# Performance work log

Hardware: AMD Instinct MI355X
Metric: run time of the kernel (lower is better)

## Reference

```python
import jax, jax.numpy as jnp
import numpy as np

B, N1, N2 = 4, 2048, 8192
F_IN, F_OUT = 256, 256
K = 3          # PyG knn_interpolate default
BN_EPS = 1e-5


def linear_bn(x, W, b, gamma, beta):
    # Linear + BatchNorm1d (training mode: batch stats over B*N per feature)
    h = jnp.einsum('bni,io->bno', x, W) + b
    mean = h.mean(axis=(0, 1))
    var = h.var(axis=(0, 1))
    xhat = (h - mean) * jax.lax.rsqrt(var + BN_EPS)
    return gamma * xhat + beta


def knn_interpolate(f1, p1, p2):
    # f1: [N1,F], p1: [N1,3], p2: [N2,3] -> [N2,F]
    d2 = jnp.sum((p2[:, None, :] - p1[None, :, :]) ** 2, axis=-1)  # [N2,N1]
    neg_d2, idx = jax.lax.top_k(-d2, K)                            # k smallest
    w = 1.0 / jnp.maximum(-neg_d2, 1e-16)                          # [N2,K]
    fk = f1[idx]                                                   # [N2,K,F]
    return jnp.sum(w[..., None] * fk, axis=1) / jnp.sum(w, axis=1, keepdims=True)


def setup_inputs() -> dict:
    key = jax.random.key(0)
    ks = jax.random.split(key, 10)
    return {
        'features_1': jax.random.normal(ks[0], (B, N1, F_IN), jnp.float32),
        'positions_1': jax.random.uniform(ks[1], (B, N1, 3), jnp.float32),
        'batch_1': jnp.repeat(jnp.arange(B, dtype=jnp.int64), N1),
        'features_2': jax.random.normal(ks[2], (B, N2, F_IN), jnp.float32),
        'positions_2': jax.random.uniform(ks[3], (B, N2, 3), jnp.float32),
        'batch_2': jnp.repeat(jnp.arange(B, dtype=jnp.int64), N2),
        'W1': jax.random.normal(ks[4], (F_IN, F_OUT), jnp.float32) * (1.0 / np.sqrt(F_IN)),
        'b1': jax.random.normal(ks[5], (F_OUT,), jnp.float32) * 0.02,
        'gamma1': jnp.ones((F_OUT,), jnp.float32),
        'beta1': jnp.zeros((F_OUT,), jnp.float32),
        'W2': jax.random.normal(ks[6], (F_IN, F_OUT), jnp.float32) * (1.0 / np.sqrt(F_IN)),
        'b2': jax.random.normal(ks[7], (F_OUT,), jnp.float32) * 0.02,
        'gamma2': jnp.ones((F_OUT,), jnp.float32),
        'beta2': jnp.zeros((F_OUT,), jnp.float32),
    }


def reference(features_1, positions_1, batch_1, features_2, positions_2, batch_2,
              W1, b1, gamma1, beta1, W2, b2, gamma2, beta2):
    f1 = linear_bn(features_1, W1, b1, gamma1, beta1)          # [B,N1,F_OUT]
    f2 = linear_bn(features_2, W2, b2, gamma2, beta2)          # [B,N2,F_OUT]
    # batch structure is regular [B,N]: knn restricted within batch == vmap over B
    interp = jax.vmap(knn_interpolate)(f1, positions_1, positions_2)  # [B,N2,F_OUT]
    return (interp + f2, positions_2, batch_2)
```

## Files before the change

### kernel.cpp

```cpp
#include <hip/hip_runtime.h>
#include <math.h>

#define BATCH   4
#define N1      2048
#define N2      8192
#define F       256
#define NTOT1   (BATCH * N1)
#define NTOT2   (BATCH * N2)
#define BN_EPS  1e-5f

#define GR      6
#define NC      216
#define NCP     (NC + 1)
#define GH      (1.0f / 6.0f)

typedef __attribute__((ext_vector_type(8))) short bf16x8;
typedef __attribute__((ext_vector_type(8))) unsigned short u16x8;
typedef __attribute__((ext_vector_type(4))) float f32x4;

__device__ __forceinline__ unsigned short f2bf(float f) {
    unsigned u = __float_as_uint(f);
    unsigned r = (u + 0x7fffu + ((u >> 16) & 1u)) >> 16;
    return (unsigned short)r;
}
__device__ __forceinline__ float bflo(unsigned u) {
    return __uint_as_float(u << 16);
}
__device__ __forceinline__ float bfhi(unsigned u) {
    return __uint_as_float(u & 0xffff0000u);
}
__device__ __forceinline__ void async16(const void* g, void* l) {
    __builtin_amdgcn_global_load_lds(
        (const __attribute__((address_space(1))) unsigned int*)g,
        (__attribute__((address_space(3))) unsigned int*)l, 16, 0, 0);
}

__device__ __forceinline__ void ins3m(float d, int j,
                                      float& d0, float& d1, float& d2,
                                      int& j0, int& j1, int& j2) {
    const bool c0 = d < d0;
    const bool c1 = d < d1;
    const bool c2 = d < d2;
    const float nd1 = __builtin_amdgcn_fmed3f(d, d0, d1);
    const float nd2 = __builtin_amdgcn_fmed3f(d, d1, d2);
    d0 = fminf(d, d0);
    d1 = nd1;
    d2 = nd2;
    j2 = c1 ? j1 : (c2 ? j : j2);
    j1 = c0 ? j0 : (c1 ? j : j1);
    j0 = c0 ? j  : j0;
}

__device__ __forceinline__ int clamp6(int c) { return c < 0 ? 0 : (c > 5 ? 5 : c); }
__device__ __forceinline__ int cell_of(float x, float y, float z) {
    const int cx = clamp6((int)(x * 6.0f));
    const int cy = clamp6((int)(y * 6.0f));
    const int cz = clamp6((int)(z * 6.0f));
    return (cz * 6 + cy) * 6 + cx;
}

__global__ __launch_bounds__(256) void prep_kernel(const float* __restrict__ W1,
                                                   const float* __restrict__ W2,
                                                   unsigned short* __restrict__ Wt1,
                                                   unsigned short* __restrict__ Wt2,
                                                   float* __restrict__ sums) {
    const int bx = blockIdx.x;
    const int t  = threadIdx.x;

    if (bx < 32) {
        __shared__ float tile[64][65];
        const bool second = bx >= 16;
        const int bl = second ? bx - 16 : bx;
        const float* W = second ? W2 : W1;
        unsigned short* Wt = second ? Wt2 : Wt1;
        const int gx0 = (bl & 3) * 64;
        const int gy0 = (bl >> 2) * 64;
        const int tx = t & 63;
        const int ty = t >> 6;
        #pragma unroll
        for (int j = 0; j < 16; ++j) {
            const int row = ty * 16 + j;
            tile[row][tx] = W[(size_t)(gy0 + row) * 256 + gx0 + tx];
        }
        __syncthreads();
        #pragma unroll
        for (int j = 0; j < 16; ++j) {
            const int row = ty * 16 + j;
            Wt[(size_t)(gx0 + row) * 256 + gy0 + tx] = f2bf(tile[tx][row]);
        }
    } else {
        #pragma unroll
        for (int i = 0; i < 4; ++i) sums[t + 256 * i] = 0.0f;
    }
}

__global__ __launch_bounds__(256) void gemm_mfma_kernel(const float* __restrict__ f1,
                                                        const float* __restrict__ f2,
                                                        const unsigned short* __restrict__ Wt1,
                                                        const unsigned short* __restrict__ Wt2,
                                                        const float* __restrict__ b1,
                                                        const float* __restrict__ b2,
                                                        const float* __restrict__ p1,
                                                        const float* __restrict__ p2,
                                                        unsigned short* __restrict__ h1b,
                                                        unsigned short* __restrict__ h2b,
                                                        float* __restrict__ sums,
                                                        float4* __restrict__ gridPts,
                                                        int* __restrict__ cellStart,
                                                        int* __restrict__ qSorted,
                                                        int* __restrict__ qCellStart) {
    __shared__ unsigned short As[128 * 32];
    __shared__ unsigned short Bs[128 * 32];

    const int bx = blockIdx.x;
    const int t  = threadIdx.x;

    if (bx >= 640) {
        __shared__ int cnt[NC];
        __shared__ int ofs[NCP];
        __shared__ unsigned char cellb[N2];
        const int bb = bx - 640;
        if (bb < 4) {
            const int b = bb;
            if (t < NC) cnt[t] = 0;
            __syncthreads();
            int   myc[8];
            float mx[8], my[8], mz[8];
            #pragma unroll
            for (int r = 0; r < 8; ++r) {
                const int i = r * 256 + t;
                const size_t base = (size_t)(b * N1 + i) * 3;
                mx[r] = p1[base]; my[r] = p1[base + 1]; mz[r] = p1[base + 2];
                myc[r] = cell_of(mx[r], my[r], mz[r]);
                atomicAdd(&cnt[myc[r]], 1);
            }
            __syncthreads();
            if (t <= NC) ofs[t] = (t == 0) ? 0 : cnt[t - 1];
            __syncthreads();
            for (int dd = 1; dd < NCP; dd <<= 1) {
                int v = 0;
                if (t <= NC && t >= dd) v = ofs[t - dd];
                __syncthreads();
                if (t <= NC && t >= dd) ofs[t] += v;
                __syncthreads();
            }
            if (t < NC) cnt[t] = ofs[t];
            __syncthreads();
            #pragma unroll
            for (int r = 0; r < 8; ++r) {
                const int i = r * 256 + t;
                const int pos = atomicAdd(&cnt[myc[r]], 1);
                float4 rec;
                rec.x = mx[r]; rec.y = my[r]; rec.z = mz[r];
                rec.w = __int_as_float(i);
                gridPts[(size_t)b * N1 + pos] = rec;
            }
            if (t <= NC) cellStart[b * NCP + t] = ofs[t];
        } else {
            const int b = bb - 4;
            if (t < NC) cnt[t] = 0;
            __syncthreads();
            for (int r = 0; r < 32; ++r) {
                const int i = r * 256 + t;
                const size_t base = (size_t)(b * N2 + i) * 3;
                const int c = cell_of(p2[base], p2[base + 1], p2[base + 2]);
                cellb[i] = (unsigned char)c;
                atomicAdd(&cnt[c], 1);
            }
            __syncthreads();
            if (t <= NC) ofs[t] = (t == 0) ? 0 : cnt[t - 1];
            __syncthreads();
            for (int dd = 1; dd < NCP; dd <<= 1) {
                int v = 0;
                if (t <= NC && t >= dd) v = ofs[t - dd];
                __syncthreads();
                if (t <= NC && t >= dd) ofs[t] += v;
                __syncthreads();
            }
            if (t < NC) cnt[t] = ofs[t];
            __syncthreads();
            for (int r = 0; r < 32; ++r) {
                const int i = r * 256 + t;
                const int c = cellb[i];
                const int pos = atomicAdd(&cnt[c], 1);
                qSorted[(size_t)b * N2 + pos] = b * N2 + i;
            }
            if (t <= NC) qCellStart[b * NCP + t] = ofs[t];
        }
        return;
    }

    const int L  = (bx & 7) * 80 + (bx >> 3);
    const bool g2 = L >= 128;
    const int ll  = g2 ? L - 128 : L;
    const int mb  = ll >> 1;
    const int nbi = ll & 1;

    const float* Fsrc        = g2 ? f2 : f1;
    const unsigned short* Wt = g2 ? Wt2 : Wt1;
    const float* bias        = g2 ? b2 : b1;
    unsigned short* Hb       = g2 ? h2b : h1b;
    float* sum               = sums + (g2 ? 512 : 0);
    float* sumsq             = sum + 256;
    const int row0 = mb * 128;
    const int n0   = nbi * 128;

    const int wave = t >> 6;
    const int lane = t & 63;
    const int wm   = (wave & 1) * 64;
    const int wn   = (wave >> 1) * 64;
    const int ml   = lane & 15;
    const int q    = lane >> 4;

    float4 arA[2], arB[2];
    auto loadA = [&](int kt) {
        #pragma unroll
        for (int i = 0; i < 2; ++i) {
            const int pi  = i * 256 + t;
            const int row = pi >> 2;
            const int q2  = pi & 3;
            const float4* src = (const float4*)Fsrc
                              + (size_t)(row0 + row) * 64 + kt * 8 + q2 * 2;
            arA[i] = src[0];
            arB[i] = src[1];
        }
    };
    auto writeA = [&]() {
        #pragma unroll
        for (int i = 0; i < 2; ++i) {
            const int pi  = i * 256 + t;
            const int row = pi >> 2;
            const int q2  = pi & 3;
            u16x8 v;
            v[0] = f2bf(arA[i].x); v[1] = f2bf(arA[i].y);
            v[2] = f2bf(arA[i].z); v[3] = f2bf(arA[i].w);
            v[4] = f2bf(arB[i].x); v[5] = f2bf(arB[i].y);
            v[6] = f2bf(arB[i].z); v[7] = f2bf(arB[i].w);
            *(u16x8*)&As[row * 32 + q2 * 8] = v;
        }
    };
    auto stageB = [&](int kt) {
        #pragma unroll
        for (int r = 0; r < 2; ++r) {
            const int e   = r * 2048 + t * 8;
            const int row = e >> 5;
            const int kk  = e & 31;
            async16(Wt + (size_t)(n0 + row) * 256 + kt * 32 + kk,
                    (unsigned short*)Bs + e);
        }
    };

    f32x4 acc[4][4] = {};

    loadA(0);
    stageB(0);
    writeA();
    loadA(1);
    __syncthreads();

    for (int kt = 0; kt < 8; ++kt) {
        bf16x8 af[4], bfr[4];
        #pragma unroll
        for (int mt = 0; mt < 4; ++mt)
            af[mt] = *(const bf16x8*)&As[(wm + mt * 16 + ml) * 32 + q * 8];
        #pragma unroll
        for (int nt = 0; nt < 4; ++nt)
            bfr[nt] = *(const bf16x8*)&Bs[(wn + nt * 16 + ml) * 32 + q * 8];
        #pragma unroll
        for (int mt = 0; mt < 4; ++mt)
            #pragma unroll
            for (int nt = 0; nt < 4; ++nt)
                acc[mt][nt] = __builtin_amdgcn_mfma_f32_16x16x32_bf16(af[mt], bfr[nt],
                                                                      acc[mt][nt], 0, 0, 0);
        if (kt < 7) {
            __syncthreads();
            stageB(kt + 1);
            writeA();
            if (kt < 6) loadA(kt + 2);
            __syncthreads();
        }
    }

    float bv[4], psum[4], psq[4];
    #pragma unroll
    for (int nt = 0; nt < 4; ++nt) {
        bv[nt] = bias[n0 + wn + nt * 16 + ml];
        psum[nt] = 0.0f; psq[nt] = 0.0f;
    }
    #pragma unroll
    for (int mt = 0; mt < 4; ++mt)
        #pragma unroll
        for (int nt = 0; nt < 4; ++nt)
            #pragma unroll
            for (int r = 0; r < 4; ++r) {
                const float v = acc[mt][nt][r] + bv[nt];
                const int grow = row0 + wm + mt * 16 + q * 4 + r;
                Hb[(size_t)grow * 256 + n0 + wn + nt * 16 + ml] = f2bf(v);
                psum[nt] += v;
                psq[nt]  = fmaf(v, v, psq[nt]);
            }
    #pragma unroll
    for (int nt = 0; nt < 4; ++nt) {
        psum[nt] += __shfl_xor(psum[nt], 16, 64);
        psum[nt] += __shfl_xor(psum[nt], 32, 64);
        psq[nt]  += __shfl_xor(psq[nt], 16, 64);
        psq[nt]  += __shfl_xor(psq[nt], 32, 64);
    }
    if (q == 0) {
        #pragma unroll
        for (int nt = 0; nt < 4; ++nt) {
            const int col = n0 + wn + nt * 16 + ml;
            atomicAdd(&sum[col],   psum[nt]);
            atomicAdd(&sumsq[col], psq[nt]);
        }
    }
}

__global__ __launch_bounds__(512) void fused_kernel(const float* __restrict__ p2,
                                                    const unsigned short* __restrict__ h1b,
                                                    const unsigned short* __restrict__ h2b,
                                                    const float* __restrict__ sums,
                                                    const float* __restrict__ g1,
                                                    const float* __restrict__ be1,
                                                    const float* __restrict__ g2,
                                                    const float* __restrict__ be2,
                                                    const float4* __restrict__ gridPts,
                                                    const int* __restrict__ cellStart,
                                                    const int* __restrict__ qSorted,
                                                    const int* __restrict__ qCellStart,
                                                    float* __restrict__ out) {
    __shared__ float ssl[4][256];
    __shared__ int   cst[NCP];
    __shared__ float pdl[8][64][3];
    __shared__ int   pil[8][64][3];
    __shared__ float qdl[64][3];
    __shared__ int   qjl[64][3];
    __shared__ float wql[64][3];
    __shared__ int   jql[64][3];
    __shared__ int   qidl[64];
    __shared__ float qpx[64], qpy[64], qpz[64];

    const int t    = threadIdx.x;
    const int bx   = blockIdx.x;
    const int b    = bx / NC;
    const int cid  = bx - b * NC;
    const int ccx  = cid % 6;
    const int ccy  = (cid / 6) % 6;
    const int ccz  = cid / 36;
    const int wave = t >> 6;
    const int lane = t & 63;

    if (t < 256) {
        const float m1 = sums[t] * (1.0f / (float)NTOT1);
        const float v1 = sums[256 + t] * (1.0f / (float)NTOT1) - m1 * m1;
        const float s1 = g1[t] * rsqrtf(v1 + BN_EPS);
        ssl[0][t] = s1;
        ssl[1][t] = be1[t] - m1 * s1;
        const float m2 = sums[512 + t] * (1.0f / (float)NTOT2);
        const float v2 = sums[768 + t] * (1.0f / (float)NTOT2) - m2 * m2;
        const float s2 = g2[t] * rsqrtf(v2 + BN_EPS);
        ssl[2][t] = s2;
        ssl[3][t] = be2[t] - m2 * s2;
    }
    if (t < NCP) cst[t] = cellStart[b * NCP + t];

    const int qs = qCellStart[b * NCP + cid];
    const int qe = qCellStart[b * NCP + cid + 1];
    const float4* __restrict__ gp = gridPts + (size_t)b * N1;

    for (int q0 = qs; q0 < qe; q0 += 64) {
        const int nqc = min(64, qe - q0);
        __syncthreads();
        if (t < 64) {
            int qid = 0;
            float x = 1e30f, y = 1e30f, z = 1e30f;
            if (t < nqc) {
                qid = qSorted[(size_t)b * N2 + q0 + t];
                const size_t pb = (size_t)qid * 3;
                x = p2[pb]; y = p2[pb + 1]; z = p2[pb + 2];
            }
            qidl[t] = qid;
            qpx[t] = x; qpy[t] = y; qpz[t] = z;
        }
        __syncthreads();

        const float qx = qpx[lane], qy = qpy[lane], qz = qpz[lane];

        auto scan_box = [&](int R, float& d0, float& d1, float& d2,
                            int& i0, int& i1, int& i2) {
            const int dim  = 2 * R + 1;
            const int dim2 = dim * dim;
            const int nsl  = dim2 * dim;
            for (int sl = wave; sl < nsl; sl += 8) {
                int lz = sl / dim2;
                const int rem = sl - lz * dim2;
                int ly = rem / dim;
                int lx = rem - ly * dim;
                lx -= R; ly -= R; lz -= R;
                if (R > 1) {
                    const int ax = lx < 0 ? -lx : lx;
                    const int ay = ly < 0 ? -ly : ly;
                    const int az = lz < 0 ? -lz : lz;
                    int ch = ax > ay ? ax : ay;
                    ch = ch > az ? ch : az;
                    if (ch < R) continue;
                }
                const int gx = ccx + lx;
                const int gy = ccy + ly;
                const int gz = ccz + lz;
                if ((unsigned)gx >= 6u || (unsigned)gy >= 6u || (unsigned)gz >= 6u)
                    continue;
                const int cc = (gz * 6 + gy) * 6 + gx;
                const int s = __builtin_amdgcn_readfirstlane(cst[cc]);
                const int e = __builtin_amdgcn_readfirstlane(cst[cc + 1]);
                for (int j = s; j < e; ++j) {
                    const float4 p = gp[j];
                    const float dx = p.x - qx;
                    const float dy = p.y - qy;
                    const float dz = p.z - qz;
                    float d = dx * dx;
                    d = fmaf(dy, dy, d);
                    d = fmaf(dz, dz, d);
                    ins3m(d, __float_as_int(p.w), d0, d1, d2, i0, i1, i2);
                }
            }
        };

        auto merge_check = [&](int R) -> int {
            int notdone = 0;
            if (t < 64) {
                float m0, m1, m2;
                int a0, a1, a2;
                if (R == 1) { m0 = m1 = m2 = 1e30f; a0 = a1 = a2 = 0; }
                else {
                    m0 = qdl[t][0]; m1 = qdl[t][1]; m2 = qdl[t][2];
                    a0 = qjl[t][0]; a1 = qjl[t][1]; a2 = qjl[t][2];
                }
                #pragma unroll
                for (int s = 0; s < 8; ++s)
                    #pragma unroll
                    for (int k = 0; k < 3; ++k)
                        ins3m(pdl[s][t][k], pil[s][t][k], m0, m1, m2, a0, a1, a2);
                qdl[t][0] = m0; qdl[t][1] = m1; qdl[t][2] = m2;
                qjl[t][0] = a0; qjl[t][1] = a1; qjl[t][2] = a2;
                if (t < nqc) {
                    float dmin = 1e30f;
                    {
                        const int lo = ccx - R, hi = ccx + R;
                        if (lo > 0) dmin = fminf(dmin, qpx[t] - (float)lo * GH);
                        if (hi < 5) dmin = fminf(dmin, (float)(hi + 1) * GH - qpx[t]);
                    }
                    {
                        const int lo = ccy - R, hi = ccy + R;
                        if (lo > 0) dmin = fminf(dmin, qpy[t] - (float)lo * GH);
                        if (hi < 5) dmin = fminf(dmin, (float)(hi + 1) * GH - qpy[t]);
                    }
                    {
                        const int lo = ccz - R, hi = ccz + R;
                        if (lo > 0) dmin = fminf(dmin, qpz[t] - (float)lo * GH);
                        if (hi < 5) dmin = fminf(dmin, (float)(hi + 1) * GH - qpz[t]);
                    }
                    if (m2 > dmin * dmin * 0.9999f) notdone = 1;
                }
            }
            return __syncthreads_count(notdone);
        };

        {
            float d0 = 1e30f, d1 = 1e30f, d2 = 1e30f;
            int i0 = 0, i1 = 0, i2 = 0;
            scan_box(1, d0, d1, d2, i0, i1, i2);
            pdl[wave][lane][0] = d0; pdl[wave][lane][1] = d1; pdl[wave][lane][2] = d2;
            pil[wave][lane][0] = i0; pil[wave][lane][1] = i1; pil[wave][lane][2] = i2;
        }
        __syncthreads();
        int need = merge_check(1);
        for (int R = 2; need != 0 && R <= 6; ++R) {
            float d0 = 1e30f, d1 = 1e30f, d2 = 1e30f;
            int i0 = 0, i1 = 0, i2 = 0;
            scan_box(R, d0, d1, d2, i0, i1, i2);
            pdl[wave][lane][0] = d0; pdl[wave][lane][1] = d1; pdl[wave][lane][2] = d2;
            pil[wave][lane][0] = i0; pil[wave][lane][1] = i1; pil[wave][lane][2] = i2;
            __syncthreads();
            need = merge_check(R);
        }

        if (t < nqc) {
            const float w0 = 1.0f / fmaxf(qdl[t][0], 1e-16f);
            const float w1 = 1.0f / fmaxf(qdl[t][1], 1e-16f);
            const float w2 = 1.0f / fmaxf(qdl[t][2], 1e-16f);
            const float inv = 1.0f / (w0 + w1 + w2);
            wql[t][0] = w0 * inv; wql[t][1] = w1 * inv; wql[t][2] = w2 * inv;
            jql[t][0] = b * N1 + qjl[t][0];
            jql[t][1] = b * N1 + qjl[t][1];
            jql[t][2] = b * N1 + qjl[t][2];
        }
        __syncthreads();

        {
            const int fp = t & 127;
            const int f0 = fp * 2;
            const float s1a = ssl[0][f0],     t1a = ssl[1][f0];
            const float s2a = ssl[2][f0],     t2a = ssl[3][f0];
            const float s1b = ssl[0][f0 + 1], t1b = ssl[1][f0 + 1];
            const float s2b = ssl[2][f0 + 1], t2b = ssl[3][f0 + 1];
            for (int v = t >> 7; v < nqc; v += 4) {
                const int qid = qidl[v];
                const int   j0 = jql[v][0], j1 = jql[v][1], j2 = jql[v][2];
                const float w0 = wql[v][0], w1 = wql[v][1], w2 = wql[v][2];

                const unsigned u0 = *(const unsigned*)(h1b + (size_t)j0 * F + f0);
                const unsigned u1 = *(const unsigned*)(h1b + (size_t)j1 * F + f0);
                const unsigned u2 = *(const unsigned*)(h1b + (size_t)j2 * F + f0);
                const unsigned uh = *(const unsigned*)(h2b + (size_t)qid * F + f0);

                float alo = w0 * bflo(u0);
                alo = fmaf(w1, bflo(u1), alo);
                alo = fmaf(w2, bflo(u2), alo);
                float ahi = w0 * bfhi(u0);
                ahi = fmaf(w1, bfhi(u1), ahi);
                ahi = fmaf(w2, bfhi(u2), ahi);

                float2 o;
                o.x = fmaf(alo, s1a, t1a) + fmaf(bflo(uh), s2a, t2a);
                o.y = fmaf(ahi, s1b, t1b) + fmaf(bfhi(uh), s2b, t2b);
                *(float2*)(out + (size_t)qid * F + f0) = o;
            }
        }
    }

    if (t < 152) {
        const int tid = bx * 152 + t;
        if (tid < NTOT2 * 3) {
            out[(size_t)NTOT2 * F + tid] = p2[tid];
        } else if (tid < NTOT2 * 3 + NTOT2) {
            const int e = tid - NTOT2 * 3;
            out[(size_t)NTOT2 * F + NTOT2 * 3 + e] = (float)(e >> 13);
        }
    }
}

extern "C" void kernel_launch(void* const* d_in, const int* in_sizes, int n_in,
                              void* d_out, int out_size, void* d_ws, size_t ws_size,
                              hipStream_t stream) {
    const float* f1  = (const float*)d_in[0];
    const float* p1  = (const float*)d_in[1];
    const float* f2  = (const float*)d_in[3];
    const float* p2  = (const float*)d_in[4];
    const float* W1  = (const float*)d_in[6];
    const float* b1  = (const float*)d_in[7];
    const float* g1  = (const float*)d_in[8];
    const float* be1 = (const float*)d_in[9];
    const float* W2  = (const float*)d_in[10];
    const float* b2  = (const float*)d_in[11];
    const float* g2  = (const float*)d_in[12];
    const float* be2 = (const float*)d_in[13];

    char* ws = (char*)d_ws;
    unsigned short* Wt1   = (unsigned short*)(ws);
    unsigned short* Wt2   = (unsigned short*)(ws + 131072);
    unsigned short* h1b   = (unsigned short*)(ws + 262144);
    unsigned short* h2b   = (unsigned short*)(ws + 4456448);
    float*          sums  = (float*)(ws + 21233664);
    float4*         gridPts    = (float4*)(ws + 21237760);
    int*            cellStart  = (int*)(ws + 21368832);
    int*            qSorted    = (int*)(ws + 21372416);
    int*            qCellStart = (int*)(ws + 21503488);
    float*          out   = (float*)d_out;

    prep_kernel<<<33, 256, 0, stream>>>(W1, W2, Wt1, Wt2, sums);

    gemm_mfma_kernel<<<648, 256, 0, stream>>>(f1, f2, Wt1, Wt2, b1, b2, p1, p2,
                                              h1b, h2b, sums,
                                              gridPts, cellStart, qSorted, qCellStart);

    fused_kernel<<<864, 512, 0, stream>>>(p2, h1b, h2b, sums,
                                          g1, be1, g2, be2,
                                          gridPts, cellStart, qSorted, qCellStart,
                                          out);
}
```

Baseline: 161.8 us.

## Load A fragments directly to registers and double-buffer B tiles in LDS

The GEMM no longer stages the A tile through shared memory. Each lane loads the fp32 rows it needs straight from global memory into registers, converts them to bf16, and feeds them to MFMA, with the next k-step's loads issued ahead. The B tile is double-buffered in LDS, cutting the per-step barriers from two to one. This removes LDS writes and reads for A and some synchronization, but every wave reloads its A rows (duplicated global reads across the two N-waves) and register pressure goes up.

```diff
diff --git a/kernel.cpp b/kernel.cpp
--- a/kernel.cpp
+++ b/kernel.cpp
@@ -109,8 +109,7 @@
                                                         int* __restrict__ cellStart,
                                                         int* __restrict__ qSorted,
                                                         int* __restrict__ qCellStart) {
-    __shared__ unsigned short As[128 * 32];
-    __shared__ unsigned short Bs[128 * 32];
+    __shared__ unsigned short Bs[2][128 * 32];
 
     const int bx = blockIdx.x;
     const int t  = threadIdx.x;
@@ -212,74 +211,72 @@
     const int ml   = lane & 15;
     const int q    = lane >> 4;
 
-    float4 arA[2], arB[2];
-    auto loadA = [&](int kt) {
-        #pragma unroll
-        for (int i = 0; i < 2; ++i) {
-            const int pi  = i * 256 + t;
-            const int row = pi >> 2;
-            const int q2  = pi & 3;
-            const float4* src = (const float4*)Fsrc
-                              + (size_t)(row0 + row) * 64 + kt * 8 + q2 * 2;
-            arA[i] = src[0];
-            arB[i] = src[1];
-        }
-    };
-    auto writeA = [&]() {
-        #pragma unroll
-        for (int i = 0; i < 2; ++i) {
-            const int pi  = i * 256 + t;
-            const int row = pi >> 2;
-            const int q2  = pi & 3;
-            u16x8 v;
-            v[0] = f2bf(arA[i].x); v[1] = f2bf(arA[i].y);
-            v[2] = f2bf(arA[i].z); v[3] = f2bf(arA[i].w);
-            v[4] = f2bf(arB[i].x); v[5] = f2bf(arB[i].y);
-            v[6] = f2bf(arB[i].z); v[7] = f2bf(arB[i].w);
-            *(u16x8*)&As[row * 32 + q2 * 8] = v;
-        }
-    };
-    auto stageB = [&](int kt) {
+    auto stageB = [&](int kt, int buf) {
         #pragma unroll
         for (int r = 0; r < 2; ++r) {
             const int e   = r * 2048 + t * 8;
             const int row = e >> 5;
             const int kk  = e & 31;
             async16(Wt + (size_t)(n0 + row) * 256 + kt * 32 + kk,
-                    (unsigned short*)Bs + e);
+                    (unsigned short*)Bs[buf] + e);
         }
     };
+    auto loadA = [&](int kt, float4 (&dst)[8]) {
+        #pragma unroll
+        for (int mt = 0; mt < 4; ++mt) {
+            const float4* ap = (const float4*)Fsrc
+                             + (size_t)(row0 + wm + mt * 16 + ml) * 64 + kt * 8 + q * 2;
+            dst[2 * mt]     = ap[0];
+            dst[2 * mt + 1] = ap[1];
+        }
+    };
+    auto cvtA = [&](const float4 (&src)[8], bf16x8 (&af)[4]) {
+        #pragma unroll
+        for (int mt = 0; mt < 4; ++mt) {
+            u16x8 v;
+            v[0] = f2bf(src[2 * mt].x);     v[1] = f2bf(src[2 * mt].y);
+            v[2] = f2bf(src[2 * mt].z);     v[3] = f2bf(src[2 * mt].w);
+            v[4] = f2bf(src[2 * mt + 1].x); v[5] = f2bf(src[2 * mt + 1].y);
+            v[6] = f2bf(src[2 * mt + 1].z); v[7] = f2bf(src[2 * mt + 1].w);
+            af[mt] = *(const bf16x8*)&v;
+        }
+    };
 
     f32x4 acc[4][4] = {};
-
-    loadA(0);
-    stageB(0);
-    writeA();
-    loadA(1);
+    float4 arP[8], arQ[8];
+
+    stageB(0, 0);
+    loadA(0, arP);
     __syncthreads();
 
-    for (int kt = 0; kt < 8; ++kt) {
-        bf16x8 af[4], bfr[4];
-        #pragma unroll
-        for (int mt = 0; mt < 4; ++mt)
-            af[mt] = *(const bf16x8*)&As[(wm + mt * 16 + ml) * 32 + q * 8];
-        #pragma unroll
-        for (int nt = 0; nt < 4; ++nt)
-            bfr[nt] = *(const bf16x8*)&Bs[(wn + nt * 16 + ml) * 32 + q * 8];
-        #pragma unroll
-        for (int mt = 0; mt < 4; ++mt)
-            #pragma unroll
-            for (int nt = 0; nt < 4; ++nt)
-                acc[mt][nt] = __builtin_amdgcn_mfma_f32_16x16x32_bf16(af[mt], bfr[nt],
-                                                                      acc[mt][nt], 0, 0, 0);
-        if (kt < 7) {
-            __syncthreads();
-            stageB(kt + 1);
-            writeA();
-            if (kt < 6) loadA(kt + 2);
-            __syncthreads();
-        }
-    }
+#define GEMM_STEP(KT, CURA, NXTA, CBUF)                                        \
+    {                                                                          \
+        if ((KT) < 7) stageB((KT) + 1, (CBUF) ^ 1);           \
+        if ((KT) < 7) loadA((KT) + 1, NXTA);                  \
+        bf16x8 af[4];                                                          \
+        cvtA(CURA, af);                                                        \
+        bf16x8 bfr[4];                                                         \
+        _Pragma("unroll")                                                      \
+        for (int nt = 0; nt < 4; ++nt)                                         \
+            bfr[nt] = *(const bf16x8*)&Bs[CBUF][(wn + nt * 16 + ml) * 32 + q * 8]; \
+        _Pragma("unroll")                                                      \
+        for (int mt = 0; mt < 4; ++mt)                                         \
+            _Pragma("unroll")                                                  \
+            for (int nt = 0; nt < 4; ++nt)                                     \
+                acc[mt][nt] = __builtin_amdgcn_mfma_f32_16x16x32_bf16(         \
+                    af[mt], bfr[nt], acc[mt][nt], 0, 0, 0);                    \
+        if ((KT) < 7) __syncthreads();    \
+    }
+
+    GEMM_STEP(0, arP, arQ, 0)
+    GEMM_STEP(1, arQ, arP, 1)
+    GEMM_STEP(2, arP, arQ, 0)
+    GEMM_STEP(3, arQ, arP, 1)
+    GEMM_STEP(4, arP, arQ, 0)
+    GEMM_STEP(5, arQ, arP, 1)
+    GEMM_STEP(6, arP, arQ, 0)
+    GEMM_STEP(7, arQ, arP, 1)
+#undef GEMM_STEP
 
     float bv[4], psum[4], psq[4];
     #pragma unroll
```

Result: slower. 169.4 us (+4.7%).
